# Kernel optimization log

Measured on AMD Instinct MI355X. Metric: run time of the kernel, lower is better.

Reference implementation:

```python
import jax, jax.numpy as jnp
import numpy as np

B, H, Q, D = 2, 8, 4096, 32
GH, GW = 32, 32  # key grid height/width


def setup_inputs() -> dict:
    key = jax.random.key(0)
    k1, k2, k3, k4 = jax.random.split(key, 4)
    queries = jax.random.normal(k1, (B, H, Q, D), dtype=jnp.float32)
    keys = jax.random.normal(k2, (B, H, GH, GW, D), dtype=jnp.float32)
    pos = jax.random.randint(k3, (B, Q, 2), 0, GH)  # integer (y, x) grid position of each query
    rel_bias = jax.random.normal(k4, (H, 2 * GH - 1, 2 * GW - 1), dtype=jnp.float32)
    return {"queries": queries, "keys": keys, "pos": pos, "rel_bias": rel_bias}


def reference(queries, keys, pos, rel_bias):
    # queries: [B,H,Q,D]; keys: [B,H,GH,GW,D]; pos: [B,Q,2] int; rel_bias: [H,2GH-1,2GW-1]
    b, h, q, d = queries.shape
    gh, gw = keys.shape[2], keys.shape[3]
    scale = 1.0 / jnp.sqrt(jnp.asarray(d, queries.dtype))
    # attention scores against every grid cell: [B,H,Q,GH,GW]
    scores = jnp.einsum('bhqd,bhijd->bhqij', queries, keys) * scale
    # relative offset indices into the bias table
    rel_y = jnp.arange(gh)[None, None, :] - pos[..., 0][..., None] + (gh - 1)  # [B,Q,GH]
    rel_x = jnp.arange(gw)[None, None, :] - pos[..., 1][..., None] + (gw - 1)  # [B,Q,GW]
    # gather per-head bias: [H,B,Q,GH,GW] -> [B,H,Q,GH,GW]
    bias = rel_bias[:, rel_y[:, :, :, None], rel_x[:, :, None, :]]
    bias = jnp.transpose(bias, (1, 0, 2, 3, 4))
    logits = scores + bias
    attn = jax.nn.softmax(logits.reshape(b, h, q, gh * gw), axis=-1)
    return attn.reshape(b, h, q, gh, gw)
```

## Files before the change

### kernel.cpp

```cpp
#include <hip/hip_runtime.h>

namespace {
constexpr int B_ = 2, H_ = 8, Q_ = 4096, D_ = 32;
constexpr int NPOS = 1024;
constexpr int NB = 63;
constexpr int NT = 256;
constexpr int TILES_PER_WAVE = 2;
constexpr int QCHUNK = 16 * 4 * TILES_PER_WAVE;
constexpr float SCALE = 0.17677669529663687f;
constexpr float LOG2E = 1.4426950408889634f;
constexpr float C1 = SCALE * LOG2E;
}

typedef __attribute__((ext_vector_type(8))) short short8;
typedef __attribute__((ext_vector_type(4))) float float4v;

__device__ __forceinline__ unsigned short f2bf(float f) {
  unsigned u = __float_as_uint(f);
  u += 0x7fffu + ((u >> 16) & 1u);
  return (unsigned short)(u >> 16);
}

__device__ __forceinline__ float fexp2(float x) {
#if defined(__has_builtin)
#if __has_builtin(__builtin_amdgcn_exp2f)
  return __builtin_amdgcn_exp2f(x);
#else
  return exp2f(x);
#endif
#else
  return exp2f(x);
#endif
}

__device__ __forceinline__ float frcp(float x) {
#if defined(__has_builtin)
#if __has_builtin(__builtin_amdgcn_rcpf)
  return __builtin_amdgcn_rcpf(x);
#else
  return 1.0f / x;
#endif
#else
  return 1.0f / x;
#endif
}

__device__ __forceinline__ unsigned pack_hi16(unsigned hi_from, unsigned lo_from) {
#if defined(__has_builtin)
#if __has_builtin(__builtin_amdgcn_perm)
  return __builtin_amdgcn_perm(hi_from, lo_from, 0x07060302u);
#else
  return (lo_from >> 16) | (hi_from & 0xffff0000u);
#endif
#else
  return (lo_from >> 16) | (hi_from & 0xffff0000u);
#endif
}

__global__ __launch_bounds__(NT, 2)
void rga_kernel(const float* __restrict__ queries,
                const float* __restrict__ keys,
                const int*   __restrict__ pos,
                const float* __restrict__ rel_bias,
                float* __restrict__ out) {
  __shared__ __align__(16) unsigned short klds[NPOS * D_];

  const int t    = threadIdx.x;
  const int lane = t & 63;
  const int w    = t >> 6;
  const int m    = lane & 15;
  const int quad = lane >> 4;
  const int h  = blockIdx.y;
  const int b  = blockIdx.z;
  const int bh = b * H_ + h;
  const int q0 = blockIdx.x * QCHUNK;

  {
    const float4* src = (const float4*)(keys + (size_t)bh * NPOS * D_);
    #pragma unroll
    for (int i = 0; i < (NPOS * D_ / 4) / NT; ++i) {
      float4 v = src[i * NT + t];
      unsigned lo = (unsigned)f2bf(v.x) | ((unsigned)f2bf(v.y) << 16);
      unsigned hi = (unsigned)f2bf(v.z) | ((unsigned)f2bf(v.w) << 16);
      ((uint2*)klds)[i * NT + t] = make_uint2(lo, hi);
    }
  }
  __syncthreads();

  const float* bias_h = rel_bias + (size_t)h * (NB * NB);

  for (int ti = 0; ti < TILES_PER_WAVE; ++ti) {
    const int qt0 = q0 + (w * TILES_PER_WAVE + ti) * 16;

    short8 afrag;
    {
      const float* qrow = queries + ((size_t)(bh * Q_ + qt0 + m)) * D_ + quad * 8;
      float4 x = *(const float4*)(qrow);
      float4 y = *(const float4*)(qrow + 4);
      afrag[0] = (short)f2bf(x.x); afrag[1] = (short)f2bf(x.y);
      afrag[2] = (short)f2bf(x.z); afrag[3] = (short)f2bf(x.w);
      afrag[4] = (short)f2bf(y.x); afrag[5] = (short)f2bf(y.y);
      afrag[6] = (short)f2bf(y.z); afrag[7] = (short)f2bf(y.w);
    }

    const float* bptr0; const float* bptr1; const float* bptr2; const float* bptr3;
    {
      const int2* pp = (const int2*)(pos + ((size_t)b * Q_ + qt0 + quad * 4) * 2);
      int2 p0 = pp[0], p1 = pp[1], p2 = pp[2], p3 = pp[3];
      bptr0 = bias_h + (31 - p0.x) * NB + (31 - p0.y) + m;
      bptr1 = bias_h + (31 - p1.x) * NB + (31 - p1.y) + m;
      bptr2 = bias_h + (31 - p2.x) * NB + (31 - p2.y) + m;
      bptr3 = bias_h + (31 - p3.x) * NB + (31 - p3.y) + m;
    }

    float sum0 = 0.f, sum1 = 0.f, sum2 = 0.f, sum3 = 0.f;
    unsigned Epk[2 * (NPOS / 16)];

    #pragma unroll
    for (int n = 0; n < NPOS / 16; ++n) {
      const short8 bfrag =
          *(const short8*)(klds + (size_t)(n * 16 + m) * D_ + quad * 8);
      float4v acc = __builtin_amdgcn_mfma_f32_16x16x32_bf16(
          afrag, bfrag, (float4v){0.f, 0.f, 0.f, 0.f}, 0, 0, 0);
      const int doff = (n >> 1) * NB + ((n & 1) << 4);
      float e0 = fexp2(acc[0] * C1 + bptr0[doff] * LOG2E);
      float e1 = fexp2(acc[1] * C1 + bptr1[doff] * LOG2E);
      float e2 = fexp2(acc[2] * C1 + bptr2[doff] * LOG2E);
      float e3 = fexp2(acc[3] * C1 + bptr3[doff] * LOG2E);
      sum0 += e0; sum1 += e1; sum2 += e2; sum3 += e3;
      Epk[2 * n]     = pack_hi16(__float_as_uint(e1), __float_as_uint(e0));
      Epk[2 * n + 1] = pack_hi16(__float_as_uint(e3), __float_as_uint(e2));
    }

    #pragma unroll
    for (int mask = 1; mask <= 8; mask <<= 1) {
      sum0 += __shfl_xor(sum0, mask, 64);
      sum1 += __shfl_xor(sum1, mask, 64);
      sum2 += __shfl_xor(sum2, mask, 64);
      sum3 += __shfl_xor(sum3, mask, 64);
    }
    const float r0 = frcp(sum0), r1 = frcp(sum1), r2 = frcp(sum2), r3 = frcp(sum3);

    float* o0 = out + ((size_t)(bh * Q_ + qt0 + quad * 4)) * NPOS + m;
    float* o1 = o0 + NPOS;
    float* o2 = o1 + NPOS;
    float* o3 = o2 + NPOS;
    #pragma unroll
    for (int n = 0; n < NPOS / 16; ++n) {
      unsigned ua = Epk[2 * n], ub = Epk[2 * n + 1];
      o0[n * 16] = __uint_as_float(ua << 16) * r0;
      o1[n * 16] = __uint_as_float(ua & 0xffff0000u) * r1;
      o2[n * 16] = __uint_as_float(ub << 16) * r2;
      o3[n * 16] = __uint_as_float(ub & 0xffff0000u) * r3;
    }
  }
}

extern "C" void kernel_launch(void* const* d_in, const int* in_sizes, int n_in,
                              void* d_out, int out_size, void* d_ws, size_t ws_size,
                              hipStream_t stream) {
  const float* queries  = (const float*)d_in[0];
  const float* keys     = (const float*)d_in[1];
  const int*   pos      = (const int*)d_in[2];
  const float* rel_bias = (const float*)d_in[3];
  float* out = (float*)d_out;

  dim3 grid(Q_ / QCHUNK, H_, B_);
  dim3 block(NT);
  hipLaunchKernelGGL(rga_kernel, grid, block, 0, stream,
                     queries, keys, pos, rel_bias, out);
}
```

Before: 304.8 us.

## Swap MFMA operands, recompute scores in a second pass, use vector nontemporal stores

The MFMA operands are swapped so each lane holds four consecutive key columns of a single query row. That lets the bias be read as a float4 and the output written with 16-byte nontemporal stores. The exponentials are no longer kept in registers as packed bf16. A second pass redoes the MFMA and exp after the row sum is known, which also drops the bf16 rounding of the output. The block grows to 512 threads with one tile per wave, cutting register pressure, at the cost of twice the MFMA and exp work.

Result: slower. 339.5 us (+11.4%).

```diff
diff --git a/kernel.cpp b/kernel.cpp
--- a/kernel.cpp
+++ b/kernel.cpp
@@ -4,9 +4,8 @@
 constexpr int B_ = 2, H_ = 8, Q_ = 4096, D_ = 32;
 constexpr int NPOS = 1024;
 constexpr int NB = 63;
-constexpr int NT = 256;
-constexpr int TILES_PER_WAVE = 2;
-constexpr int QCHUNK = 16 * 4 * TILES_PER_WAVE;
+constexpr int NT = 512;
+constexpr int QCHUNK = 128;
 constexpr float SCALE = 0.17677669529663687f;
 constexpr float LOG2E = 1.4426950408889634f;
 constexpr float C1 = SCALE * LOG2E;
@@ -45,19 +44,7 @@
 #endif
 }
 
-__device__ __forceinline__ unsigned pack_hi16(unsigned hi_from, unsigned lo_from) {
-#if defined(__has_builtin)
-#if __has_builtin(__builtin_amdgcn_perm)
-  return __builtin_amdgcn_perm(hi_from, lo_from, 0x07060302u);
-#else
-  return (lo_from >> 16) | (hi_from & 0xffff0000u);
-#endif
-#else
-  return (lo_from >> 16) | (hi_from & 0xffff0000u);
-#endif
-}
-
-__global__ __launch_bounds__(NT, 2)
+__global__ __launch_bounds__(NT, 4)
 void rga_kernel(const float* __restrict__ queries,
                 const float* __restrict__ keys,
                 const int*   __restrict__ pos,
@@ -76,7 +63,7 @@
   const int q0 = blockIdx.x * QCHUNK;
 
   {
-    const float4* src = (const float4*)(keys + (size_t)bh * NPOS * D_);
+    const float4* src = (const float4*)(keys + (size_t)bh * (NPOS * D_));
     #pragma unroll
     for (int i = 0; i < (NPOS * D_ / 4) / NT; ++i) {
       float4 v = src[i * NT + t];
@@ -87,72 +74,60 @@
   }
   __syncthreads();
 
-  const float* bias_h = rel_bias + (size_t)h * (NB * NB);
+  const int qrow = q0 + w * 16 + m;
 
-  for (int ti = 0; ti < TILES_PER_WAVE; ++ti) {
-    const int qt0 = q0 + (w * TILES_PER_WAVE + ti) * 16;
+  short8 afrag;
+  {
+    const float* qp = queries + ((size_t)(bh * Q_) + qrow) * D_ + quad * 8;
+    float4 x = *(const float4*)(qp);
+    float4 y = *(const float4*)(qp + 4);
+    afrag[0] = (short)f2bf(x.x); afrag[1] = (short)f2bf(x.y);
+    afrag[2] = (short)f2bf(x.z); afrag[3] = (short)f2bf(x.w);
+    afrag[4] = (short)f2bf(y.x); afrag[5] = (short)f2bf(y.y);
+    afrag[6] = (short)f2bf(y.z); afrag[7] = (short)f2bf(y.w);
+  }
 
-    short8 afrag;
-    {
-      const float* qrow = queries + ((size_t)(bh * Q_ + qt0 + m)) * D_ + quad * 8;
-      float4 x = *(const float4*)(qrow);
-      float4 y = *(const float4*)(qrow + 4);
-      afrag[0] = (short)f2bf(x.x); afrag[1] = (short)f2bf(x.y);
-      afrag[2] = (short)f2bf(x.z); afrag[3] = (short)f2bf(x.w);
-      afrag[4] = (short)f2bf(y.x); afrag[5] = (short)f2bf(y.y);
-      afrag[6] = (short)f2bf(y.z); afrag[7] = (short)f2bf(y.w);
-    }
+  const float* bbase;
+  {
+    int2 p = *(const int2*)(pos + ((size_t)b * Q_ + qrow) * 2);
+    bbase = rel_bias + (size_t)h * (NB * NB)
+          + (31 - p.x) * NB + (31 - p.y) + quad * 4;
+  }
 
-    const float* bptr0; const float* bptr1; const float* bptr2; const float* bptr3;
-    {
-      const int2* pp = (const int2*)(pos + ((size_t)b * Q_ + qt0 + quad * 4) * 2);
-      int2 p0 = pp[0], p1 = pp[1], p2 = pp[2], p3 = pp[3];
-      bptr0 = bias_h + (31 - p0.x) * NB + (31 - p0.y) + m;
-      bptr1 = bias_h + (31 - p1.x) * NB + (31 - p1.y) + m;
-      bptr2 = bias_h + (31 - p2.x) * NB + (31 - p2.y) + m;
-      bptr3 = bias_h + (31 - p3.x) * NB + (31 - p3.y) + m;
-    }
+  const unsigned short* kbase = klds + m * D_ + quad * 8;
 
-    float sum0 = 0.f, sum1 = 0.f, sum2 = 0.f, sum3 = 0.f;
-    unsigned Epk[2 * (NPOS / 16)];
+  float sum = 0.f;
+  #pragma unroll
+  for (int n = 0; n < NPOS / 16; ++n) {
+    const short8 kf = *(const short8*)(kbase + n * 512);
+    float4v acc = __builtin_amdgcn_mfma_f32_16x16x32_bf16(
+        kf, afrag, (float4v){0.f, 0.f, 0.f, 0.f}, 0, 0, 0);
+    float4v bv;
+    __builtin_memcpy(&bv, bbase + (n >> 1) * NB + ((n & 1) << 4), 16);
+    float e0 = fexp2(acc[0] * C1 + bv[0] * LOG2E);
+    float e1 = fexp2(acc[1] * C1 + bv[1] * LOG2E);
+    float e2 = fexp2(acc[2] * C1 + bv[2] * LOG2E);
+    float e3 = fexp2(acc[3] * C1 + bv[3] * LOG2E);
+    sum += (e0 + e1) + (e2 + e3);
+  }
+  sum += __shfl_xor(sum, 16, 64);
+  sum += __shfl_xor(sum, 32, 64);
+  const float rinv = frcp(sum);
 
-    #pragma unroll
-    for (int n = 0; n < NPOS / 16; ++n) {
-      const short8 bfrag =
-          *(const short8*)(klds + (size_t)(n * 16 + m) * D_ + quad * 8);
-      float4v acc = __builtin_amdgcn_mfma_f32_16x16x32_bf16(
-          afrag, bfrag, (float4v){0.f, 0.f, 0.f, 0.f}, 0, 0, 0);
-      const int doff = (n >> 1) * NB + ((n & 1) << 4);
-      float e0 = fexp2(acc[0] * C1 + bptr0[doff] * LOG2E);
-      float e1 = fexp2(acc[1] * C1 + bptr1[doff] * LOG2E);
-      float e2 = fexp2(acc[2] * C1 + bptr2[doff] * LOG2E);
-      float e3 = fexp2(acc[3] * C1 + bptr3[doff] * LOG2E);
-      sum0 += e0; sum1 += e1; sum2 += e2; sum3 += e3;
-      Epk[2 * n]     = pack_hi16(__float_as_uint(e1), __float_as_uint(e0));
-      Epk[2 * n + 1] = pack_hi16(__float_as_uint(e3), __float_as_uint(e2));
-    }
-
-    #pragma unroll
-    for (int mask = 1; mask <= 8; mask <<= 1) {
-      sum0 += __shfl_xor(sum0, mask, 64);
-      sum1 += __shfl_xor(sum1, mask, 64);
-      sum2 += __shfl_xor(sum2, mask, 64);
-      sum3 += __shfl_xor(sum3, mask, 64);
-    }
-    const float r0 = frcp(sum0), r1 = frcp(sum1), r2 = frcp(sum2), r3 = frcp(sum3);
-
-    float* o0 = out + ((size_t)(bh * Q_ + qt0 + quad * 4)) * NPOS + m;
-    float* o1 = o0 + NPOS;
-    float* o2 = o1 + NPOS;
-    float* o3 = o2 + NPOS;
-    #pragma unroll
-    for (int n = 0; n < NPOS / 16; ++n) {
-      unsigned ua = Epk[2 * n], ub = Epk[2 * n + 1];
-      o0[n * 16] = __uint_as_float(ua << 16) * r0;
-      o1[n * 16] = __uint_as_float(ua & 0xffff0000u) * r1;
-      o2[n * 16] = __uint_as_float(ub << 16) * r2;
-      o3[n * 16] = __uint_as_float(ub & 0xffff0000u) * r3;
-    }
+  float* orow = out + ((size_t)(bh * Q_) + qrow) * NPOS + quad * 4;
+  #pragma unroll
+  for (int n = 0; n < NPOS / 16; ++n) {
+    const short8 kf = *(const short8*)(kbase + n * 512);
+    float4v acc = __builtin_amdgcn_mfma_f32_16x16x32_bf16(
+        kf, afrag, (float4v){0.f, 0.f, 0.f, 0.f}, 0, 0, 0);
+    float4v bv;
+    __builtin_memcpy(&bv, bbase + (n >> 1) * NB + ((n & 1) << 4), 16);
+    float4v ev;
+    ev[0] = fexp2(acc[0] * C1 + bv[0] * LOG2E) * rinv;
+    ev[1] = fexp2(acc[1] * C1 + bv[1] * LOG2E) * rinv;
+    ev[2] = fexp2(acc[2] * C1 + bv[2] * LOG2E) * rinv;
+    ev[3] = fexp2(acc[3] * C1 + bv[3] * LOG2E) * rinv;
+    __builtin_nontemporal_store(ev, (float4v*)(orow + n * 16));
   }
 }
 
```
